# Kernel tuning notes

Hardware: AMD Instinct MI355X
Metric: run time of the kernel (lower is better)

Reference implementation:

```python
import jax, jax.numpy as jnp
import numpy as np

D_IN, D_OUT, N_TOK = 4096, 4096, 8192

def _binarize(w):
    # sign with straight-through estimator (sign(0) treated as sign output of jnp.sign)
    return w + jax.lax.stop_gradient(jnp.sign(w) - w)

def setup_inputs() -> dict:
    key = jax.random.key(0)
    k1, k2, k3, k4, k5 = jax.random.split(key, 5)
    x = jax.random.normal(k1, (N_TOK, D_IN), dtype=jnp.float32)
    W1 = jax.random.normal(k2, (D_OUT, D_IN), dtype=jnp.float32)
    W2 = jax.random.normal(k3, (D_OUT, D_IN), dtype=jnp.float32)
    b1 = jax.random.normal(k4, (D_OUT,), dtype=jnp.float32)
    b2 = jax.random.normal(k5, (D_OUT,), dtype=jnp.float32)
    return {"x": x, "W1": W1, "W2": W2, "b1": b1, "b2": b2}

def reference(x, W1, W2, b1, b2):
    # BinaryLinear: F.linear(x, sign(W), b); TernaryLinear = binary1(x) - binary2(x)
    out1 = x @ _binarize(W1).T + b1
    out2 = x @ _binarize(W2).T + b2
    return out1 - out2
```

## Files before the change

kernel.cpp:

```cpp
#include <hip/hip_runtime.h>


#define DIM_K 4096
#define DIM_N 4096
#define DIM_M 8192

typedef _Float16 f16x8 __attribute__((ext_vector_type(8)));
typedef float    f32x4 __attribute__((ext_vector_type(4)));


__device__ __forceinline__ float signdiff(float a, float b) {
    const float sa = (float)((a > 0.f) - (a < 0.f));
    const float sb = (float)((b > 0.f) - (b < 0.f));
    return sa - sb;
}

__global__ void cvt_fused(const float4* __restrict__ x,
                          const float4* __restrict__ w1,
                          const float4* __restrict__ w2,
                          f16x8* __restrict__ xh,
                          f16x8* __restrict__ wh) {
    const int XU = DIM_M * DIM_K / 8;
    const int TU = XU + DIM_N * DIM_K / 8;
    const int stride = gridDim.x * blockDim.x;
    for (int u = blockIdx.x * blockDim.x + threadIdx.x; u < TU; u += stride) {
        if (u < XU) {
            const float4 a = x[2 * u], b = x[2 * u + 1];
            f16x8 h;
            h[0] = (_Float16)a.x; h[1] = (_Float16)a.y;
            h[2] = (_Float16)a.z; h[3] = (_Float16)a.w;
            h[4] = (_Float16)b.x; h[5] = (_Float16)b.y;
            h[6] = (_Float16)b.z; h[7] = (_Float16)b.w;
            xh[u] = h;
        } else {
            const int v = u - XU;
            const float4 a1 = w1[2 * v], b1 = w1[2 * v + 1];
            const float4 a2 = w2[2 * v], b2 = w2[2 * v + 1];
            f16x8 h;
            h[0] = (_Float16)signdiff(a1.x, a2.x);
            h[1] = (_Float16)signdiff(a1.y, a2.y);
            h[2] = (_Float16)signdiff(a1.z, a2.z);
            h[3] = (_Float16)signdiff(a1.w, a2.w);
            h[4] = (_Float16)signdiff(b1.x, b2.x);
            h[5] = (_Float16)signdiff(b1.y, b2.y);
            h[6] = (_Float16)signdiff(b1.z, b2.z);
            h[7] = (_Float16)signdiff(b1.w, b2.w);
            wh[v] = h;
        }
    }
}


__global__ __launch_bounds__(512, 2) void ternary_gemm(
    const _Float16* __restrict__ Xh, const _Float16* __restrict__ Wh,
    const float* __restrict__ B1, const float* __restrict__ B2,
    float* __restrict__ C) {
    __shared__ __align__(16) char smem[131072];

    const int tid  = threadIdx.x;
    const int wave = tid >> 6;
    const int lane = tid & 63;
    const int wm = wave >> 2;
    const int wn = wave & 3;
    const int q  = lane >> 4;
    const int r  = lane & 15;

    const int bid = blockIdx.x;
    const int id  = (bid & 7) * 64 + (bid >> 3);
    const int bRowM = (id >> 4) * 256;
    const int bColN = (id & 15) * 256;

    const int srow   = tid >> 3;
    const int gchunk = (tid & 7) ^ (srow & 7);
    const char* aSrc = (const char*)Xh + (size_t)(bRowM + srow) * (DIM_K * 2) + gchunk * 16;
    const char* bSrc = (const char*)Wh + (size_t)(bColN + srow) * (DIM_K * 2) + gchunk * 16;
    char* const ldsBase = smem;
    const int waveOff = wave * 1024;

#define STAGE_A(bufsel, h, dk) do {                                                             \
    _Pragma("unroll")                                                                           \
    for (int i_ = 0; i_ < 2; ++i_)                                                              \
        __builtin_amdgcn_global_load_lds(                                                       \
            (const __attribute__((address_space(1))) void*)(                                    \
                aSrc + (size_t)((h) * 128 + i_ * 64) * (DIM_K * 2) + (dk) * 128),               \
            (__attribute__((address_space(3))) void*)(                                          \
                ldsBase + (bufsel) * 32768 + ((h) * 128 + i_ * 64) * 128 + waveOff),            \
            16, 0, 0);                                                                          \
} while (0)
#define STAGE_B(bufsel, h, dk) do {                                                             \
    _Pragma("unroll")                                                                           \
    for (int i_ = 0; i_ < 2; ++i_)                                                              \
        __builtin_amdgcn_global_load_lds(                                                       \
            (const __attribute__((address_space(1))) void*)(                                    \
                bSrc + (size_t)((h) * 128 + i_ * 64) * (DIM_K * 2) + (dk) * 128),               \
            (__attribute__((address_space(3))) void*)(                                          \
                ldsBase + 65536 + (bufsel) * 32768 + ((h) * 128 + i_ * 64) * 128 + waveOff),    \
            16, 0, 0);                                                                          \
} while (0)

    const int swz = r & 7;
    char* const aRd = smem + (wm * 64 + r) * 128;
    char* const bRd = smem + 65536 + (wn * 32 + r) * 128;
    const int ck0 = ((0 * 4 + q) ^ swz) * 16;
    const int ck1 = ((1 * 4 + q) ^ swz) * 16;

    f32x4 acc[2][2][4][2] = {};
    f16x8 af[4][2], bf0[2][2], bf1[2][2];

    STAGE_A(0, 0, 0);
    STAGE_B(0, 0, 0);
    STAGE_A(0, 1, 0);
    STAGE_B(0, 1, 0);
    STAGE_A(1, 0, 1);
    STAGE_B(1, 0, 1);
    asm volatile("s_waitcnt vmcnt(4)" ::: "memory");
    __builtin_amdgcn_s_barrier();
    __builtin_amdgcn_sched_barrier(0);

    for (int kt = 0; kt < 64; ++kt) {
        const int cur = kt & 1, nxt = cur ^ 1;
        const char* const aC = aRd + cur * 32768;
        const char* const bC = bRd + cur * 32768;

#pragma unroll
        for (int im = 0; im < 4; ++im) {
            af[im][0] = *(const f16x8*)(aC + im * 2048 + ck0);
            af[im][1] = *(const f16x8*)(aC + im * 2048 + ck1);
        }
#pragma unroll
        for (int in = 0; in < 2; ++in) {
            bf0[in][0] = *(const f16x8*)(bC + in * 2048 + ck0);
            bf0[in][1] = *(const f16x8*)(bC + in * 2048 + ck1);
        }
        if (kt < 63) STAGE_A(nxt, 1, 1);
        __builtin_amdgcn_s_barrier();
        asm volatile("s_waitcnt lgkmcnt(0)" ::: "memory");
        __builtin_amdgcn_sched_barrier(0);
        __builtin_amdgcn_s_setprio(1);
#pragma unroll
        for (int im = 0; im < 4; ++im)
#pragma unroll
            for (int in = 0; in < 2; ++in)
#pragma unroll
                for (int kk = 0; kk < 2; ++kk)
                    acc[0][0][im][in] = __builtin_amdgcn_mfma_f32_16x16x32_f16(
                        af[im][kk], bf0[in][kk], acc[0][0][im][in], 0, 0, 0);
        __builtin_amdgcn_s_setprio(0);
        __builtin_amdgcn_sched_barrier(0);
        __builtin_amdgcn_s_barrier();
        __builtin_amdgcn_sched_barrier(0);

#pragma unroll
        for (int in = 0; in < 2; ++in) {
            bf1[in][0] = *(const f16x8*)(bC + 16384 + in * 2048 + ck0);
            bf1[in][1] = *(const f16x8*)(bC + 16384 + in * 2048 + ck1);
        }
        if (kt < 63) STAGE_B(nxt, 1, 1);
        __builtin_amdgcn_s_barrier();
        asm volatile("s_waitcnt lgkmcnt(0)" ::: "memory");
        __builtin_amdgcn_sched_barrier(0);
        __builtin_amdgcn_s_setprio(1);
#pragma unroll
        for (int im = 0; im < 4; ++im)
#pragma unroll
            for (int in = 0; in < 2; ++in)
#pragma unroll
                for (int kk = 0; kk < 2; ++kk)
                    acc[0][1][im][in] = __builtin_amdgcn_mfma_f32_16x16x32_f16(
                        af[im][kk], bf1[in][kk], acc[0][1][im][in], 0, 0, 0);
        __builtin_amdgcn_s_setprio(0);
        __builtin_amdgcn_sched_barrier(0);
        __builtin_amdgcn_s_barrier();
        __builtin_amdgcn_sched_barrier(0);

#pragma unroll
        for (int im = 0; im < 4; ++im) {
            af[im][0] = *(const f16x8*)(aC + 16384 + im * 2048 + ck0);
            af[im][1] = *(const f16x8*)(aC + 16384 + im * 2048 + ck1);
        }
        if (kt < 62) STAGE_A(cur, 0, 2);
        __builtin_amdgcn_s_barrier();
        asm volatile("s_waitcnt lgkmcnt(0)" ::: "memory");
        __builtin_amdgcn_sched_barrier(0);
        __builtin_amdgcn_s_setprio(1);
#pragma unroll
        for (int im = 0; im < 4; ++im)
#pragma unroll
            for (int in = 0; in < 2; ++in)
#pragma unroll
                for (int kk = 0; kk < 2; ++kk)
                    acc[1][0][im][in] = __builtin_amdgcn_mfma_f32_16x16x32_f16(
                        af[im][kk], bf0[in][kk], acc[1][0][im][in], 0, 0, 0);
        __builtin_amdgcn_s_setprio(0);
        __builtin_amdgcn_sched_barrier(0);
        __builtin_amdgcn_s_barrier();
        __builtin_amdgcn_sched_barrier(0);

        if (kt < 62) STAGE_B(cur, 0, 2);
        __builtin_amdgcn_s_barrier();
        __builtin_amdgcn_s_setprio(1);
#pragma unroll
        for (int im = 0; im < 4; ++im)
#pragma unroll
            for (int in = 0; in < 2; ++in)
#pragma unroll
                for (int kk = 0; kk < 2; ++kk)
                    acc[1][1][im][in] = __builtin_amdgcn_mfma_f32_16x16x32_f16(
                        af[im][kk], bf1[in][kk], acc[1][1][im][in], 0, 0, 0);
        __builtin_amdgcn_s_setprio(0);
        if (kt < 62) {
            asm volatile("s_waitcnt vmcnt(4)" ::: "memory");
        } else if (kt == 62) {
            asm volatile("s_waitcnt vmcnt(0)" ::: "memory");
        }
        __builtin_amdgcn_s_barrier();
        __builtin_amdgcn_sched_barrier(0);

        aSrc += 128;
        bSrc += 128;
    }

#pragma unroll
    for (int nh = 0; nh < 2; ++nh) {
#pragma unroll
        for (int in = 0; in < 2; ++in) {
            const int col = bColN + nh * 128 + wn * 32 + in * 16 + r;
            const float bia = B1[col] - B2[col];
#pragma unroll
            for (int mh = 0; mh < 2; ++mh) {
#pragma unroll
                for (int im = 0; im < 4; ++im) {
                    const int row0 = bRowM + mh * 128 + wm * 64 + im * 16 + q * 4;
                    const f32x4 v = acc[mh][nh][im][in];
#pragma unroll
                    for (int j = 0; j < 4; ++j)
                        C[(size_t)(row0 + j) * DIM_N + col] = v[j] + bia;
                }
            }
        }
    }
#undef STAGE_A
#undef STAGE_B
}


extern "C" void kernel_launch(void* const* d_in, const int* in_sizes, int n_in,
                              void* d_out, int out_size, void* d_ws, size_t ws_size,
                              hipStream_t stream) {
    const float* x  = (const float*)d_in[0];
    const float* W1 = (const float*)d_in[1];
    const float* W2 = (const float*)d_in[2];
    const float* b1 = (const float*)d_in[3];
    const float* b2 = (const float*)d_in[4];
    float* out = (float*)d_out;

    _Float16* Xh = (_Float16*)d_ws;
    _Float16* Wh = (_Float16*)((char*)d_ws + (size_t)67108864);
    (void)ws_size; (void)in_sizes; (void)n_in; (void)out_size;

    cvt_fused<<<2048, 256, 0, stream>>>((const float4*)x, (const float4*)W1,
                                        (const float4*)W2, (f16x8*)Xh, (f16x8*)Wh);

    ternary_gemm<<<512, 512, 0, stream>>>(Xh, Wh, b1, b2, out);
}
```

Baseline: 527.4 us.

## Restructure GEMM main loop to overlap LDS fragment reads with MFMAs

```diff
diff --git a/kernel.cpp b/kernel.cpp
--- a/kernel.cpp
+++ b/kernel.cpp
@@ -99,120 +99,121 @@
 } while (0)
 
     const int swz = r & 7;
-    char* const aRd = smem + (wm * 64 + r) * 128;
-    char* const bRd = smem + 65536 + (wn * 32 + r) * 128;
+    const char* const aRd = smem + (wm * 64 + r) * 128;
+    const char* const bRd = smem + 65536 + (wn * 32 + r) * 128;
     const int ck0 = ((0 * 4 + q) ^ swz) * 16;
     const int ck1 = ((1 * 4 + q) ^ swz) * 16;
 
     f32x4 acc[2][2][4][2] = {};
-    f16x8 af[4][2], bf0[2][2], bf1[2][2];
-
-    STAGE_A(0, 0, 0);
-    STAGE_B(0, 0, 0);
-    STAGE_A(0, 1, 0);
-    STAGE_B(0, 1, 0);
-    STAGE_A(1, 0, 1);
-    STAGE_B(1, 0, 1);
-    asm volatile("s_waitcnt vmcnt(4)" ::: "memory");
+    f16x8 aLo[2][2], aHi[2][2], b0[2][2], b1[2][2];
+
+#define RD_ALO(base, blkoff) do {                                        \
+    aLo[0][0] = *(const f16x8*)((base) + (blkoff) + 0 * 2048 + ck0);     \
+    aLo[0][1] = *(const f16x8*)((base) + (blkoff) + 0 * 2048 + ck1);     \
+    aLo[1][0] = *(const f16x8*)((base) + (blkoff) + 1 * 2048 + ck0);     \
+    aLo[1][1] = *(const f16x8*)((base) + (blkoff) + 1 * 2048 + ck1);     \
+} while (0)
+#define RD_AHI(base, blkoff) do {                                        \
+    aHi[0][0] = *(const f16x8*)((base) + (blkoff) + 2 * 2048 + ck0);     \
+    aHi[0][1] = *(const f16x8*)((base) + (blkoff) + 2 * 2048 + ck1);     \
+    aHi[1][0] = *(const f16x8*)((base) + (blkoff) + 3 * 2048 + ck0);     \
+    aHi[1][1] = *(const f16x8*)((base) + (blkoff) + 3 * 2048 + ck1);     \
+} while (0)
+#define RD_B0(base) do {                                                 \
+    b0[0][0] = *(const f16x8*)((base) + 0 * 2048 + ck0);                 \
+    b0[0][1] = *(const f16x8*)((base) + 0 * 2048 + ck1);                 \
+    b0[1][0] = *(const f16x8*)((base) + 1 * 2048 + ck0);                 \
+    b0[1][1] = *(const f16x8*)((base) + 1 * 2048 + ck1);                 \
+} while (0)
+#define RD_B1(base) do {                                                 \
+    b1[0][0] = *(const f16x8*)((base) + 16384 + 0 * 2048 + ck0);         \
+    b1[0][1] = *(const f16x8*)((base) + 16384 + 0 * 2048 + ck1);         \
+    b1[1][0] = *(const f16x8*)((base) + 16384 + 1 * 2048 + ck0);         \
+    b1[1][1] = *(const f16x8*)((base) + 16384 + 1 * 2048 + ck1);         \
+} while (0)
+#define MM8(mh, nh, A, bb, p) do {                                       \
+    _Pragma("unroll")                                                    \
+    for (int i_ = 0; i_ < 2; ++i_)                                       \
+        _Pragma("unroll")                                                \
+        for (int n_ = 0; n_ < 2; ++n_)                                   \
+            _Pragma("unroll")                                            \
+            for (int k_ = 0; k_ < 2; ++k_)                               \
+                acc[mh][nh][(p) + i_][n_] =                              \
+                    __builtin_amdgcn_mfma_f32_16x16x32_f16(              \
+                        A[i_][k_], bb[n_][k_], acc[mh][nh][(p) + i_][n_],\
+                        0, 0, 0);                                        \
+} while (0)
+
+    STAGE_A(0, 0, 0); STAGE_A(0, 1, 0); STAGE_B(0, 0, 0); STAGE_B(0, 1, 0);
+    STAGE_A(1, 0, 1); STAGE_A(1, 1, 1); STAGE_B(1, 0, 1); STAGE_B(1, 1, 1);
+    asm volatile("s_waitcnt vmcnt(8)" ::: "memory");
     __builtin_amdgcn_s_barrier();
     __builtin_amdgcn_sched_barrier(0);
-
+    RD_B0(bRd);
+    RD_ALO(aRd, 0);
+    RD_AHI(aRd, 0);
+
+#pragma unroll 2
     for (int kt = 0; kt < 64; ++kt) {
         const int cur = kt & 1, nxt = cur ^ 1;
         const char* const aC = aRd + cur * 32768;
         const char* const bC = bRd + cur * 32768;
-
-#pragma unroll
-        for (int im = 0; im < 4; ++im) {
-            af[im][0] = *(const f16x8*)(aC + im * 2048 + ck0);
-            af[im][1] = *(const f16x8*)(aC + im * 2048 + ck1);
-        }
-#pragma unroll
-        for (int in = 0; in < 2; ++in) {
-            bf0[in][0] = *(const f16x8*)(bC + in * 2048 + ck0);
-            bf0[in][1] = *(const f16x8*)(bC + in * 2048 + ck1);
-        }
-        if (kt < 63) STAGE_A(nxt, 1, 1);
-        __builtin_amdgcn_s_barrier();
+        const char* const aN = aRd + nxt * 32768;
+        const char* const bN = bRd + nxt * 32768;
+
         asm volatile("s_waitcnt lgkmcnt(0)" ::: "memory");
         __builtin_amdgcn_sched_barrier(0);
-        __builtin_amdgcn_s_setprio(1);
-#pragma unroll
-        for (int im = 0; im < 4; ++im)
-#pragma unroll
-            for (int in = 0; in < 2; ++in)
-#pragma unroll
-                for (int kk = 0; kk < 2; ++kk)
-                    acc[0][0][im][in] = __builtin_amdgcn_mfma_f32_16x16x32_f16(
-                        af[im][kk], bf0[in][kk], acc[0][0][im][in], 0, 0, 0);
-        __builtin_amdgcn_s_setprio(0);
-        __builtin_amdgcn_sched_barrier(0);
-        __builtin_amdgcn_s_barrier();
-        __builtin_amdgcn_sched_barrier(0);
-
-#pragma unroll
-        for (int in = 0; in < 2; ++in) {
-            bf1[in][0] = *(const f16x8*)(bC + 16384 + in * 2048 + ck0);
-            bf1[in][1] = *(const f16x8*)(bC + 16384 + in * 2048 + ck1);
-        }
-        if (kt < 63) STAGE_B(nxt, 1, 1);
-        __builtin_amdgcn_s_barrier();
+        RD_B1(bC);
+        __builtin_amdgcn_s_setprio(1);
+        MM8(0, 0, aLo, b0, 0);
+        MM8(0, 0, aHi, b0, 2);
+        __builtin_amdgcn_s_setprio(0);
+        __builtin_amdgcn_sched_barrier(0);
+        __builtin_amdgcn_s_barrier();
+        __builtin_amdgcn_sched_barrier(0);
+
         asm volatile("s_waitcnt lgkmcnt(0)" ::: "memory");
         __builtin_amdgcn_sched_barrier(0);
         __builtin_amdgcn_s_setprio(1);
-#pragma unroll
-        for (int im = 0; im < 4; ++im)
-#pragma unroll
-            for (int in = 0; in < 2; ++in)
-#pragma unroll
-                for (int kk = 0; kk < 2; ++kk)
-                    acc[0][1][im][in] = __builtin_amdgcn_mfma_f32_16x16x32_f16(
-                        af[im][kk], bf1[in][kk], acc[0][1][im][in], 0, 0, 0);
-        __builtin_amdgcn_s_setprio(0);
-        __builtin_amdgcn_sched_barrier(0);
-        __builtin_amdgcn_s_barrier();
-        __builtin_amdgcn_sched_barrier(0);
-
-#pragma unroll
-        for (int im = 0; im < 4; ++im) {
-            af[im][0] = *(const f16x8*)(aC + 16384 + im * 2048 + ck0);
-            af[im][1] = *(const f16x8*)(aC + 16384 + im * 2048 + ck1);
-        }
-        if (kt < 62) STAGE_A(cur, 0, 2);
-        __builtin_amdgcn_s_barrier();
+        MM8(0, 1, aLo, b1, 0);
+        __builtin_amdgcn_s_setprio(0);
+        RD_ALO(aC, 16384);
+        __builtin_amdgcn_s_setprio(1);
+        MM8(0, 1, aHi, b1, 2);
+        __builtin_amdgcn_s_setprio(0);
+        RD_AHI(aC, 16384);
+        if (kt < 62) { STAGE_A(cur, 0, 2); STAGE_B(cur, 0, 2); }
+        __builtin_amdgcn_sched_barrier(0);
+        __builtin_amdgcn_s_barrier();
+        __builtin_amdgcn_sched_barrier(0);
+
         asm volatile("s_waitcnt lgkmcnt(0)" ::: "memory");
         __builtin_amdgcn_sched_barrier(0);
         __builtin_amdgcn_s_setprio(1);
-#pragma unroll
-        for (int im = 0; im < 4; ++im)
-#pragma unroll
-            for (int in = 0; in < 2; ++in)
-#pragma unroll
-                for (int kk = 0; kk < 2; ++kk)
-                    acc[1][0][im][in] = __builtin_amdgcn_mfma_f32_16x16x32_f16(
-                        af[im][kk], bf0[in][kk], acc[1][0][im][in], 0, 0, 0);
-        __builtin_amdgcn_s_setprio(0);
-        __builtin_amdgcn_sched_barrier(0);
-        __builtin_amdgcn_s_barrier();
-        __builtin_amdgcn_sched_barrier(0);
-
-        if (kt < 62) STAGE_B(cur, 0, 2);
-        __builtin_amdgcn_s_barrier();
-        __builtin_amdgcn_s_setprio(1);
-#pragma unroll
-        for (int im = 0; im < 4; ++im)
-#pragma unroll
-            for (int in = 0; in < 2; ++in)
-#pragma unroll
-                for (int kk = 0; kk < 2; ++kk)
-                    acc[1][1][im][in] = __builtin_amdgcn_mfma_f32_16x16x32_f16(
-                        af[im][kk], bf1[in][kk], acc[1][1][im][in], 0, 0, 0);
-        __builtin_amdgcn_s_setprio(0);
+        MM8(1, 0, aLo, b0, 0);
+        MM8(1, 0, aHi, b0, 2);
+        __builtin_amdgcn_s_setprio(0);
+        if (kt < 62) STAGE_B(cur, 1, 2);
         if (kt < 62) {
-            asm volatile("s_waitcnt vmcnt(4)" ::: "memory");
-        } else if (kt == 62) {
+            asm volatile("s_waitcnt vmcnt(6)" ::: "memory");
+        } else {
             asm volatile("s_waitcnt vmcnt(0)" ::: "memory");
         }
+        __builtin_amdgcn_sched_barrier(0);
+        __builtin_amdgcn_s_barrier();
+        __builtin_amdgcn_sched_barrier(0);
+
+        if (kt < 63) RD_B0(bN);
+        __builtin_amdgcn_s_setprio(1);
+        MM8(1, 1, aLo, b1, 0);
+        __builtin_amdgcn_s_setprio(0);
+        if (kt < 63) RD_ALO(aN, 0);
+        __builtin_amdgcn_s_setprio(1);
+        MM8(1, 1, aHi, b1, 2);
+        __builtin_amdgcn_s_setprio(0);
+        if (kt < 63) RD_AHI(aN, 0);
+        if (kt < 62) STAGE_A(cur, 1, 2);
+        __builtin_amdgcn_sched_barrier(0);
         __builtin_amdgcn_s_barrier();
         __builtin_amdgcn_sched_barrier(0);
 
@@ -241,6 +242,11 @@
     }
 #undef STAGE_A
 #undef STAGE_B
+#undef RD_ALO
+#undef RD_AHI
+#undef RD_B0
+#undef RD_B1
+#undef MM8
 }
 
 
```

New measurement: 529.9 us. No clear change (+0.5%).
